# Performance work log

Hardware: AMD Instinct MI355X
Metric: run time of the kernel (lower is better)

## Reference

```python
import jax, jax.numpy as jnp
import numpy as np

SCALE = 8.0  # sqrt(d_head=64)

def setup_inputs() -> dict:
    key = jax.random.key(0)
    kq, kk, kv = jax.random.split(key, 3)
    B, H, S, D = 2, 16, 2048, 64
    q = jax.random.normal(kq, (B, H, S, D), dtype=jnp.float32)
    k = jax.random.normal(kk, (B, H, S, D), dtype=jnp.float32)
    v = jax.random.normal(kv, (B, H, S, D), dtype=jnp.float32)
    return {"q": q, "k": k, "v": v}

def reference(q, k, v):
    # attn = softmax((q/scale) @ k^T, axis=-1); out = attn @ v
    scores = jnp.einsum('bhqd,bhkd->bhqk', q / SCALE, k)  # [B,H,S,S]
    attn = jax.nn.softmax(scores, axis=-1)
    out = jnp.einsum('bhqk,bhkd->bhqd', attn, v)          # [B,H,S,D]
    return (attn, out)
```

## Files before the change

### kernel.cpp

```cpp
#include <hip/hip_runtime.h>


#define S_LEN 2048
#define D_HEAD 64
#define QB 64
#define KB 128
#define NCHUNK (S_LEN / KB)
#define KPAD 72
#define PPAD 136
#define ATTN_ELEMS 134217728ull
#define LOG2E 1.44269504088896340736f

#define WSE_KHI 0ull
#define WSE_KLO 4194304ull
#define WSE_VT  8388608ull
#define WSE_RINV 12582912ull
#define WS_NEEDED_BYTES (12582912ull * 2ull + 65536ull * 4ull)

typedef short short8 __attribute__((ext_vector_type(8)));
typedef _Float16 half8 __attribute__((ext_vector_type(8)));
typedef float f32x16 __attribute__((ext_vector_type(16)));
typedef float floatx4 __attribute__((ext_vector_type(4)));
typedef unsigned short ushort8v __attribute__((ext_vector_type(8)));

#if __has_builtin(__builtin_amdgcn_exp2f)
#define EXP2F(x) __builtin_amdgcn_exp2f(x)
#else
#define EXP2F(x) exp2f(x)
#endif

static __device__ __forceinline__ unsigned short f2bf(float f) {
  unsigned u = __builtin_bit_cast(unsigned, f);
  u += 0x7fffu + ((u >> 16) & 1u);
  return (unsigned short)(u >> 16);
}
static __device__ __forceinline__ float bf2f(unsigned short h) {
  unsigned u = ((unsigned)h) << 16;
  return __builtin_bit_cast(float, u);
}
static __device__ __forceinline__ unsigned short f2h(float f) {
  return __builtin_bit_cast(unsigned short, (_Float16)f);
}

__global__ __launch_bounds__(512) void k_prep_k(
    const float* __restrict__ kin, unsigned short* __restrict__ khi,
    unsigned short* __restrict__ klo) {
  const size_t base = ((size_t)blockIdx.x * 512 + threadIdx.x) * 8;
  floatx4 a = *(const floatx4*)(kin + base);
  floatx4 b = *(const floatx4*)(kin + base + 4);
  ushort8v h, l;
#pragma unroll
  for (int j = 0; j < 4; ++j) {
    unsigned short ha = f2bf(a[j]); h[j] = ha; l[j] = f2bf(a[j] - bf2f(ha));
    unsigned short hb = f2bf(b[j]); h[4 + j] = hb; l[4 + j] = f2bf(b[j] - bf2f(hb));
  }
  *(ushort8v*)(khi + base) = h;
  *(ushort8v*)(klo + base) = l;
}

__global__ __launch_bounds__(512) void k_prep_v(
    const float* __restrict__ vin, unsigned short* __restrict__ vt) {
  __shared__ __align__(16) unsigned short T[64 * KPAD];
  const int tid = threadIdx.x;
  const int bh = blockIdx.x >> 3;
  const int part = blockIdx.x & 7;
  const float* V = vin + (size_t)bh * S_LEN * D_HEAD;
  unsigned short* Vt = vt + (size_t)bh * D_HEAD * S_LEN;

  const int kk_l = tid >> 3;
  const int d0 = (tid & 7) * 8;
  const int dd = tid >> 3;
  const int kb = (tid & 7) * 8;

  for (int t = part * 4; t < part * 4 + 4; ++t) {
    const int kk0 = t * 64;
    floatx4 a = *(const floatx4*)(V + (size_t)(kk0 + kk_l) * D_HEAD + d0);
    floatx4 b = *(const floatx4*)(V + (size_t)(kk0 + kk_l) * D_HEAD + d0 + 4);
#pragma unroll
    for (int j = 0; j < 4; ++j) {
      T[(d0 + j) * KPAD + kk_l] = f2h(a[j]);
      T[(d0 + 4 + j) * KPAD + kk_l] = f2h(b[j]);
    }
    __syncthreads();
    *(ushort8v*)(Vt + (size_t)dd * S_LEN + kk0 + kb) = *(const ushort8v*)&T[dd * KPAD + kb];
    __syncthreads();
  }
}

__global__ __launch_bounds__(512, 4) void k_rowsum_f(
    const float* __restrict__ q, const unsigned short* __restrict__ khi,
    const unsigned short* __restrict__ klo, float* __restrict__ rinv) {
  __shared__ float rsum_s[QB];
  const int tid = threadIdx.x;
  const int lane = tid & 63;
  const int wid = tid >> 6;
  const int rg = wid & 1, cg = wid >> 1;
  const int bxs = (blockIdx.x & 7) * 128 + (blockIdx.x >> 3);
  const int bh = bxs >> 5;
  const int qt = bxs & 31;

  const float* Q = q + (size_t)bh * S_LEN * D_HEAD;
  const unsigned short* KH = khi + (size_t)bh * S_LEN * D_HEAD;
  const unsigned short* KL = klo + (size_t)bh * S_LEN * D_HEAD;

  if (tid < QB) rsum_s[tid] = 0.0f;

  const int arow = qt * QB + rg * 32 + (lane & 31);
  const float* qp = Q + (size_t)arow * D_HEAD + ((lane >> 5) * 8);
  short8 ahi[4], alo[4];
#pragma unroll
  for (int ks = 0; ks < 4; ++ks) {
    floatx4 x0 = *(const floatx4*)(qp + ks * 16);
    floatx4 x1 = *(const floatx4*)(qp + ks * 16 + 4);
    ushort8v uh, ul;
#pragma unroll
    for (int j = 0; j < 4; ++j) {
      float xa = x0[j] * 0.125f; unsigned short ha = f2bf(xa);
      uh[j] = ha; ul[j] = f2bf(xa - bf2f(ha));
      float xb = x1[j] * 0.125f; unsigned short hb = f2bf(xb);
      uh[4 + j] = hb; ul[4 + j] = f2bf(xb - bf2f(hb));
    }
    ahi[ks] = __builtin_bit_cast(short8, uh);
    alo[ks] = __builtin_bit_cast(short8, ul);
  }

  float psum[16];
#pragma unroll
  for (int i = 0; i < 16; ++i) psum[i] = 0.0f;

  const size_t brow0 = (size_t)(cg * 32 + (lane & 31)) * D_HEAD + (lane >> 5) * 8;

  for (int ch = 0; ch < NCHUNK; ++ch) {
    const size_t cbase = (size_t)ch * KB * D_HEAD + brow0;
    f32x16 acc = {};
#pragma unroll
    for (int ks = 0; ks < 4; ++ks) {
      ushort8v bhu = *(const ushort8v*)(KH + cbase + ks * 16);
      ushort8v blu = *(const ushort8v*)(KL + cbase + ks * 16);
      short8 bh8 = __builtin_bit_cast(short8, bhu);
      short8 bl8 = __builtin_bit_cast(short8, blu);
      acc = __builtin_amdgcn_mfma_f32_32x32x16_bf16(alo[ks], bh8, acc, 0, 0, 0);
      acc = __builtin_amdgcn_mfma_f32_32x32x16_bf16(ahi[ks], bl8, acc, 0, 0, 0);
      acc = __builtin_amdgcn_mfma_f32_32x32x16_bf16(ahi[ks], bh8, acc, 0, 0, 0);
    }
#pragma unroll
    for (int i = 0; i < 16; ++i) psum[i] += EXP2F(acc[i] * LOG2E);
  }

#pragma unroll
  for (int off = 1; off < 32; off <<= 1) {
#pragma unroll
    for (int i = 0; i < 16; ++i) psum[i] += __shfl_xor(psum[i], off, 64);
  }
  if ((lane & 31) == 0) {
    const int rbase = rg * 32 + 4 * (lane >> 5);
#pragma unroll
    for (int i = 0; i < 16; ++i)
      atomicAdd(&rsum_s[rbase + (i & 3) + 8 * (i >> 2)], psum[i]);
  }
  __syncthreads();
  if (tid < QB)
    rinv[(size_t)bh * S_LEN + qt * QB + tid] = 1.0f / rsum_s[tid];
}

__global__ __launch_bounds__(512, 4) void k_attn_f(
    const float* __restrict__ q, const unsigned short* __restrict__ khi,
    const unsigned short* __restrict__ klo, const unsigned short* __restrict__ vt,
    const float* __restrict__ rinv, float* __restrict__ outbuf) {
  __shared__ __align__(16) unsigned short Pst[QB * PPAD];
  __shared__ float rinv_s[QB];

  const int tid = threadIdx.x;
  const int lane = tid & 63;
  const int wid = tid >> 6;
  const int rg = wid & 1, cg = wid >> 1;
  const int dg = (wid >> 1) & 1, kh = wid >> 2;
  const int bxs = (blockIdx.x & 7) * 128 + (blockIdx.x >> 3);
  const int bh = bxs >> 5;
  const int qt = bxs & 31;

  const float* Q = q + (size_t)bh * S_LEN * D_HEAD;
  const unsigned short* KH = khi + (size_t)bh * S_LEN * D_HEAD;
  const unsigned short* KL = klo + (size_t)bh * S_LEN * D_HEAD;
  const unsigned short* VT = vt + (size_t)bh * D_HEAD * S_LEN;
  float* attn_base = outbuf + (size_t)bh * S_LEN * S_LEN + (size_t)qt * QB * S_LEN;
  float* out_base = outbuf + ATTN_ELEMS + (size_t)bh * S_LEN * D_HEAD +
                    (size_t)qt * QB * D_HEAD;

  if (tid < QB) rinv_s[tid] = rinv[(size_t)bh * S_LEN + qt * QB + tid];

  const int arow = qt * QB + rg * 32 + (lane & 31);
  const float* qp = Q + (size_t)arow * D_HEAD + ((lane >> 5) * 8);
  short8 ahi[4], alo[4];
#pragma unroll
  for (int ks = 0; ks < 4; ++ks) {
    floatx4 x0 = *(const floatx4*)(qp + ks * 16);
    floatx4 x1 = *(const floatx4*)(qp + ks * 16 + 4);
    ushort8v uh, ul;
#pragma unroll
    for (int j = 0; j < 4; ++j) {
      float xa = x0[j] * 0.125f; unsigned short ha = f2bf(xa);
      uh[j] = ha; ul[j] = f2bf(xa - bf2f(ha));
      float xb = x1[j] * 0.125f; unsigned short hb = f2bf(xb);
      uh[4 + j] = hb; ul[4 + j] = f2bf(xb - bf2f(hb));
    }
    ahi[ks] = __builtin_bit_cast(short8, uh);
    alo[ks] = __builtin_bit_cast(short8, ul);
  }
  __syncthreads();

  floatx4 rvec[4];
  {
    const int rb = rg * 32 + 4 * (lane >> 5);
#pragma unroll
    for (int m = 0; m < 4; ++m) rvec[m] = *(const floatx4*)&rinv_s[rb + 8 * m];
  }

  f32x16 oacc = {};
  const size_t brow0 = (size_t)(cg * 32 + (lane & 31)) * D_HEAD + (lane >> 5) * 8;
  const int boff = (lane >> 5) * 8;

  for (int ch = 0; ch < NCHUNK; ++ch) {
    const int kk0 = ch * KB;
    f32x16 acc = {};
    const size_t cbase = (size_t)kk0 * D_HEAD + brow0;
#pragma unroll
    for (int ks = 0; ks < 4; ++ks) {
      ushort8v bhu = *(const ushort8v*)(KH + cbase + ks * 16);
      ushort8v blu = *(const ushort8v*)(KL + cbase + ks * 16);
      short8 bh8 = __builtin_bit_cast(short8, bhu);
      short8 bl8 = __builtin_bit_cast(short8, blu);
      acc = __builtin_amdgcn_mfma_f32_32x32x16_bf16(alo[ks], bh8, acc, 0, 0, 0);
      acc = __builtin_amdgcn_mfma_f32_32x32x16_bf16(ahi[ks], bl8, acc, 0, 0, 0);
      acc = __builtin_amdgcn_mfma_f32_32x32x16_bf16(ahi[ks], bh8, acc, 0, 0, 0);
    }
    {
      const int rbase = rg * 32 + 4 * (lane >> 5);
      const int colg = kk0 + cg * 32 + (lane & 31);
#pragma unroll
      for (int i = 0; i < 16; ++i) {
        float p = EXP2F(acc[i] * LOG2E);
        float at = p * rvec[i >> 2][i & 3];
        const int rl = rbase + (i & 3) + 8 * (i >> 2);
        __builtin_nontemporal_store(at, &attn_base[(size_t)rl * S_LEN + colg]);
        Pst[rl * PPAD + cg * 32 + (lane & 31)] = f2h(at);
      }
    }
    __syncthreads();
#pragma unroll
    for (int ks = 0; ks < 4; ++ks) {
      const int kofs = kh * 64 + ks * 16 + boff;
      ushort8v pu = *(const ushort8v*)&Pst[(rg * 32 + (lane & 31)) * PPAD + kofs];
      ushort8v vu = *(const ushort8v*)(VT + (size_t)(dg * 32 + (lane & 31)) * S_LEN + kk0 + kofs);
      oacc = __builtin_amdgcn_mfma_f32_32x32x16_f16(
          __builtin_bit_cast(half8, pu), __builtin_bit_cast(half8, vu), oacc, 0, 0, 0);
    }
    __syncthreads();
  }

  float* red = (float*)Pst;
  const int t4 = wid & 3;
  if (kh == 1) {
#pragma unroll
    for (int i = 0; i < 16; ++i) red[t4 * 1024 + i * 64 + lane] = oacc[i];
  }
  __syncthreads();
  if (kh == 0) {
#pragma unroll
    for (int i = 0; i < 16; ++i) oacc[i] += red[t4 * 1024 + i * 64 + lane];
    const int rbase = rg * 32 + 4 * (lane >> 5);
#pragma unroll
    for (int i = 0; i < 16; ++i) {
      const int rl = rbase + (i & 3) + 8 * (i >> 2);
      out_base[(size_t)rl * D_HEAD + dg * 32 + (lane & 31)] = oacc[i];
    }
  }
}

__global__ __launch_bounds__(512, 4) void k_rowsum(
    const float* __restrict__ q, const float* __restrict__ k,
    float* __restrict__ outbuf) {
  __shared__ __align__(16) unsigned short KhiS[KB * KPAD];
  __shared__ __align__(16) unsigned short KloS[KB * KPAD];
  __shared__ float rsum_s[QB];
  const int tid = threadIdx.x;
  const int lane = tid & 63;
  const int wid = tid >> 6;
  const int rg = wid & 1, cg = wid >> 1;
  const int bh = blockIdx.x >> 5;
  const int qt = blockIdx.x & 31;
  const float* Q = q + (size_t)bh * S_LEN * D_HEAD;
  const float* K = k + (size_t)bh * S_LEN * D_HEAD;
  float* rinv_out = outbuf + ATTN_ELEMS + (size_t)bh * S_LEN * D_HEAD +
                    (size_t)qt * QB * D_HEAD;
  if (tid < QB) rsum_s[tid] = 0.0f;
  const int arow = qt * QB + rg * 32 + (lane & 31);
  const float* qp = Q + (size_t)arow * D_HEAD + ((lane >> 5) * 8);
  short8 ahi[4], alo[4];
#pragma unroll
  for (int ks = 0; ks < 4; ++ks) {
    floatx4 x0 = *(const floatx4*)(qp + ks * 16);
    floatx4 x1 = *(const floatx4*)(qp + ks * 16 + 4);
    ushort8v uh, ul;
#pragma unroll
    for (int j = 0; j < 4; ++j) {
      float xa = x0[j] * 0.125f; unsigned short ha = f2bf(xa);
      uh[j] = ha; ul[j] = f2bf(xa - bf2f(ha));
      float xb = x1[j] * 0.125f; unsigned short hb = f2bf(xb);
      uh[4 + j] = hb; ul[4 + j] = f2bf(xb - bf2f(hb));
    }
    ahi[ks] = __builtin_bit_cast(short8, uh);
    alo[ks] = __builtin_bit_cast(short8, ul);
  }
  float psum[16];
#pragma unroll
  for (int i = 0; i < 16; ++i) psum[i] = 0.0f;
  const int srow = tid >> 2;
  const int scol = (tid & 3) * 16;
  const int bcol = cg * 32 + (lane & 31);
  const int boff = (lane >> 5) * 8;
  for (int ch = 0; ch < NCHUNK; ++ch) {
    const int kk0 = ch * KB;
    {
      const float* src = K + (size_t)(kk0 + srow) * D_HEAD + scol;
      floatx4 v0 = *(const floatx4*)(src);
      floatx4 v1 = *(const floatx4*)(src + 4);
      floatx4 v2 = *(const floatx4*)(src + 8);
      floatx4 v3 = *(const floatx4*)(src + 12);
      ushort8v h0, h1, l0, l1;
#pragma unroll
      for (int j = 0; j < 4; ++j) {
        unsigned short a0 = f2bf(v0[j]); h0[j] = a0; l0[j] = f2bf(v0[j] - bf2f(a0));
        unsigned short a1 = f2bf(v1[j]); h0[4+j] = a1; l0[4+j] = f2bf(v1[j] - bf2f(a1));
        unsigned short a2 = f2bf(v2[j]); h1[j] = a2; l1[j] = f2bf(v2[j] - bf2f(a2));
        unsigned short a3 = f2bf(v3[j]); h1[4+j] = a3; l1[4+j] = f2bf(v3[j] - bf2f(a3));
      }
      *(ushort8v*)&KhiS[srow * KPAD + scol] = h0;
      *(ushort8v*)&KhiS[srow * KPAD + scol + 8] = h1;
      *(ushort8v*)&KloS[srow * KPAD + scol] = l0;
      *(ushort8v*)&KloS[srow * KPAD + scol + 8] = l1;
    }
    __syncthreads();
    f32x16 acc = {};
#pragma unroll
    for (int ks = 0; ks < 4; ++ks) {
      ushort8v bhu = *(const ushort8v*)&KhiS[bcol * KPAD + ks * 16 + boff];
      ushort8v blu = *(const ushort8v*)&KloS[bcol * KPAD + ks * 16 + boff];
      short8 bh8 = __builtin_bit_cast(short8, bhu);
      short8 bl8 = __builtin_bit_cast(short8, blu);
      acc = __builtin_amdgcn_mfma_f32_32x32x16_bf16(alo[ks], bh8, acc, 0, 0, 0);
      acc = __builtin_amdgcn_mfma_f32_32x32x16_bf16(ahi[ks], bl8, acc, 0, 0, 0);
      acc = __builtin_amdgcn_mfma_f32_32x32x16_bf16(ahi[ks], bh8, acc, 0, 0, 0);
    }
#pragma unroll
    for (int i = 0; i < 16; ++i) psum[i] += EXP2F(acc[i] * LOG2E);
    __syncthreads();
  }
#pragma unroll
  for (int off = 1; off < 32; off <<= 1) {
#pragma unroll
    for (int i = 0; i < 16; ++i) psum[i] += __shfl_xor(psum[i], off, 64);
  }
  if ((lane & 31) == 0) {
    const int rbase = rg * 32 + 4 * (lane >> 5);
#pragma unroll
    for (int i = 0; i < 16; ++i)
      atomicAdd(&rsum_s[rbase + (i & 3) + 8 * (i >> 2)], psum[i]);
  }
  __syncthreads();
  if (tid < QB) rinv_out[tid] = 1.0f / rsum_s[tid];
}

__global__ __launch_bounds__(512, 4) void k_attn(
    const float* __restrict__ q, const float* __restrict__ k,
    const float* __restrict__ v, float* __restrict__ outbuf) {
  __shared__ __align__(16) unsigned short KhiS[KB * KPAD];
  __shared__ __align__(16) unsigned short KloS[KB * KPAD];
  __shared__ __align__(16) unsigned short Pst[QB * PPAD];
  __shared__ __align__(16) unsigned short VtS[D_HEAD * PPAD];
  __shared__ float rinv_s[QB];
  const int tid = threadIdx.x;
  const int lane = tid & 63;
  const int wid = tid >> 6;
  const int rg = wid & 1, cg = wid >> 1;
  const int dg = (wid >> 1) & 1, kh = wid >> 2;
  const int bh = blockIdx.x >> 5;
  const int qt = blockIdx.x & 31;
  const float* Q = q + (size_t)bh * S_LEN * D_HEAD;
  const float* K = k + (size_t)bh * S_LEN * D_HEAD;
  const float* V = v + (size_t)bh * S_LEN * D_HEAD;
  float* attn_base = outbuf + (size_t)bh * S_LEN * S_LEN + (size_t)qt * QB * S_LEN;
  float* out_base = outbuf + ATTN_ELEMS + (size_t)bh * S_LEN * D_HEAD +
                    (size_t)qt * QB * D_HEAD;
  if (tid < QB) rinv_s[tid] = out_base[tid];
  const int arow = qt * QB + rg * 32 + (lane & 31);
  const float* qp = Q + (size_t)arow * D_HEAD + ((lane >> 5) * 8);
  short8 ahi[4], alo[4];
#pragma unroll
  for (int ks = 0; ks < 4; ++ks) {
    floatx4 x0 = *(const floatx4*)(qp + ks * 16);
    floatx4 x1 = *(const floatx4*)(qp + ks * 16 + 4);
    ushort8v uh, ul;
#pragma unroll
    for (int j = 0; j < 4; ++j) {
      float xa = x0[j] * 0.125f; unsigned short ha = f2bf(xa);
      uh[j] = ha; ul[j] = f2bf(xa - bf2f(ha));
      float xb = x1[j] * 0.125f; unsigned short hb = f2bf(xb);
      uh[4 + j] = hb; ul[4 + j] = f2bf(xb - bf2f(hb));
    }
    ahi[ks] = __builtin_bit_cast(short8, uh);
    alo[ks] = __builtin_bit_cast(short8, ul);
  }
  __syncthreads();
  floatx4 rvec[4];
  {
    const int rb = rg * 32 + 4 * (lane >> 5);
#pragma unroll
    for (int m = 0; m < 4; ++m) rvec[m] = *(const floatx4*)&rinv_s[rb + 8 * m];
  }
  f32x16 oacc = {};
  const int srow = tid >> 2;
  const int scol = (tid & 3) * 16;
  const int bcol = cg * 32 + (lane & 31);
  const int boff = (lane >> 5) * 8;
  for (int ch = 0; ch < NCHUNK; ++ch) {
    const int kk0 = ch * KB;
    {
      const float* src = K + (size_t)(kk0 + srow) * D_HEAD + scol;
      floatx4 v0 = *(const floatx4*)(src);
      floatx4 v1 = *(const floatx4*)(src + 4);
      floatx4 v2 = *(const floatx4*)(src + 8);
      floatx4 v3 = *(const floatx4*)(src + 12);
      ushort8v h0, h1, l0, l1;
#pragma unroll
      for (int j = 0; j < 4; ++j) {
        unsigned short a0 = f2bf(v0[j]); h0[j] = a0; l0[j] = f2bf(v0[j] - bf2f(a0));
        unsigned short a1 = f2bf(v1[j]); h0[4+j] = a1; l0[4+j] = f2bf(v1[j] - bf2f(a1));
        unsigned short a2 = f2bf(v2[j]); h1[j] = a2; l1[j] = f2bf(v2[j] - bf2f(a2));
        unsigned short a3 = f2bf(v3[j]); h1[4+j] = a3; l1[4+j] = f2bf(v3[j] - bf2f(a3));
      }
      *(ushort8v*)&KhiS[srow * KPAD + scol] = h0;
      *(ushort8v*)&KhiS[srow * KPAD + scol + 8] = h1;
      *(ushort8v*)&KloS[srow * KPAD + scol] = l0;
      *(ushort8v*)&KloS[srow * KPAD + scol + 8] = l1;
    }
    {
#pragma unroll
      for (int half = 0; half < 2; ++half) {
        const float* vsrc = V + (size_t)(kk0 + half * 64 + wid * 8) * D_HEAD + lane;
        ushort8v hv;
#pragma unroll
        for (int i = 0; i < 8; ++i) hv[i] = f2h(vsrc[(size_t)i * D_HEAD]);
        *(ushort8v*)&VtS[lane * PPAD + half * 64 + wid * 8] = hv;
      }
    }
    __syncthreads();
    f32x16 acc = {};
#pragma unroll
    for (int ks = 0; ks < 4; ++ks) {
      ushort8v bhu = *(const ushort8v*)&KhiS[bcol * KPAD + ks * 16 + boff];
      ushort8v blu = *(const ushort8v*)&KloS[bcol * KPAD + ks * 16 + boff];
      short8 bh8 = __builtin_bit_cast(short8, bhu);
      short8 bl8 = __builtin_bit_cast(short8, blu);
      acc = __builtin_amdgcn_mfma_f32_32x32x16_bf16(alo[ks], bh8, acc, 0, 0, 0);
      acc = __builtin_amdgcn_mfma_f32_32x32x16_bf16(ahi[ks], bl8, acc, 0, 0, 0);
      acc = __builtin_amdgcn_mfma_f32_32x32x16_bf16(ahi[ks], bh8, acc, 0, 0, 0);
    }
    {
      const int rbase = rg * 32 + 4 * (lane >> 5);
      const int colg = kk0 + cg * 32 + (lane & 31);
#pragma unroll
      for (int i = 0; i < 16; ++i) {
        float p = EXP2F(acc[i] * LOG2E);
        float at = p * rvec[i >> 2][i & 3];
        const int rl = rbase + (i & 3) + 8 * (i >> 2);
        __builtin_nontemporal_store(at, &attn_base[(size_t)rl * S_LEN + colg]);
        Pst[rl * PPAD + cg * 32 + (lane & 31)] = f2h(at);
      }
    }
    __syncthreads();
#pragma unroll
    for (int ks = 0; ks < 4; ++ks) {
      const int kofs = kh * 64 + ks * 16 + boff;
      ushort8v pu = *(const ushort8v*)&Pst[(rg * 32 + (lane & 31)) * PPAD + kofs];
      ushort8v vu = *(const ushort8v*)&VtS[(dg * 32 + (lane & 31)) * PPAD + kofs];
      oacc = __builtin_amdgcn_mfma_f32_32x32x16_f16(
          __builtin_bit_cast(half8, pu), __builtin_bit_cast(half8, vu), oacc, 0, 0, 0);
    }
    __syncthreads();
  }
  float* red = (float*)KhiS;
  const int t4 = wid & 3;
  if (kh == 1) {
#pragma unroll
    for (int i = 0; i < 16; ++i) red[t4 * 1024 + i * 64 + lane] = oacc[i];
  }
  __syncthreads();
  if (kh == 0) {
#pragma unroll
    for (int i = 0; i < 16; ++i) oacc[i] += red[t4 * 1024 + i * 64 + lane];
    const int rbase = rg * 32 + 4 * (lane >> 5);
#pragma unroll
    for (int i = 0; i < 16; ++i) {
      const int rl = rbase + (i & 3) + 8 * (i >> 2);
      out_base[(size_t)rl * D_HEAD + dg * 32 + (lane & 31)] = oacc[i];
    }
  }
}

extern "C" void kernel_launch(void* const* d_in, const int* in_sizes, int n_in,
                              void* d_out, int out_size, void* d_ws, size_t ws_size,
                              hipStream_t stream) {
  const float* q = (const float*)d_in[0];
  const float* k = (const float*)d_in[1];
  const float* v = (const float*)d_in[2];
  float* out = (float*)d_out;
  (void)in_sizes; (void)n_in; (void)out_size;

  dim3 blk(512);
  if (ws_size >= WS_NEEDED_BYTES) {
    unsigned short* wsu = (unsigned short*)d_ws;
    unsigned short* khi = wsu + WSE_KHI;
    unsigned short* klo = wsu + WSE_KLO;
    unsigned short* vt = wsu + WSE_VT;
    float* rinv = (float*)(wsu + WSE_RINV);
    hipLaunchKernelGGL(k_prep_k, dim3(1024), blk, 0, stream, k, khi, klo);
    hipLaunchKernelGGL(k_prep_v, dim3(256), blk, 0, stream, v, vt);
    hipLaunchKernelGGL(k_rowsum_f, dim3(1024), blk, 0, stream, q, khi, klo, rinv);
    hipLaunchKernelGGL(k_attn_f, dim3(1024), blk, 0, stream, q, khi, klo, vt, rinv, out);
  } else {
    hipLaunchKernelGGL(k_rowsum, dim3(1024), blk, 0, stream, q, k, out);
    hipLaunchKernelGGL(k_attn, dim3(1024), blk, 0, stream, q, k, v, out);
  }
}
```

Before: 829.0 us.

## Fuse rowsum into attention kernel, merge prep kernels, use fragment-ordered K/V layouts

Merges the K and V preparation kernels into one launch and folds the row-sum pass into the attention kernel, so the attention kernel computes its own softmax normalizers before the main pass and the rinv workspace goes away. K hi/lo and V-transpose are stored in an MFMA-fragment-major layout, so each lane reads contiguous 16-byte pieces. P staging is double-buffered in shared memory, which removes one barrier per chunk and lets the attn stores overlap the PV MFMAs. This cuts launch count and workspace traffic, at the cost of more LDS per block, which could lower occupancy.

```diff
diff --git a/kernel.cpp b/kernel.cpp
--- a/kernel.cpp
+++ b/kernel.cpp
@@ -10,12 +10,12 @@
 #define PPAD 136
 #define ATTN_ELEMS 134217728ull
 #define LOG2E 1.44269504088896340736f
+#define HFRAG 131072ull
 
 #define WSE_KHI 0ull
 #define WSE_KLO 4194304ull
 #define WSE_VT  8388608ull
-#define WSE_RINV 12582912ull
-#define WS_NEEDED_BYTES (12582912ull * 2ull + 65536ull * 4ull)
+#define WS_NEEDED_BYTES (12582912ull * 2ull)
 
 typedef short short8 __attribute__((ext_vector_type(8)));
 typedef _Float16 half8 __attribute__((ext_vector_type(8)));
@@ -42,133 +42,77 @@
   return __builtin_bit_cast(unsigned short, (_Float16)f);
 }
 
-__global__ __launch_bounds__(512) void k_prep_k(
-    const float* __restrict__ kin, unsigned short* __restrict__ khi,
-    unsigned short* __restrict__ klo) {
-  const size_t base = ((size_t)blockIdx.x * 512 + threadIdx.x) * 8;
-  floatx4 a = *(const floatx4*)(kin + base);
-  floatx4 b = *(const floatx4*)(kin + base + 4);
-  ushort8v h, l;
-#pragma unroll
-  for (int j = 0; j < 4; ++j) {
-    unsigned short ha = f2bf(a[j]); h[j] = ha; l[j] = f2bf(a[j] - bf2f(ha));
-    unsigned short hb = f2bf(b[j]); h[4 + j] = hb; l[4 + j] = f2bf(b[j] - bf2f(hb));
-  }
-  *(ushort8v*)(khi + base) = h;
-  *(ushort8v*)(klo + base) = l;
-}
-
-__global__ __launch_bounds__(512) void k_prep_v(
-    const float* __restrict__ vin, unsigned short* __restrict__ vt) {
-  __shared__ __align__(16) unsigned short T[64 * KPAD];
+__global__ __launch_bounds__(512) void k_prep(
+    const float* __restrict__ kin, const float* __restrict__ vin,
+    unsigned short* __restrict__ khi, unsigned short* __restrict__ klo,
+    unsigned short* __restrict__ vt) {
+  __shared__ __align__(16) unsigned short T[64 * PPAD];
   const int tid = threadIdx.x;
-  const int bh = blockIdx.x >> 3;
-  const int part = blockIdx.x & 7;
-  const float* V = vin + (size_t)bh * S_LEN * D_HEAD;
-  unsigned short* Vt = vt + (size_t)bh * D_HEAD * S_LEN;
-
-  const int kk_l = tid >> 3;
-  const int d0 = (tid & 7) * 8;
-  const int dd = tid >> 3;
-  const int kb = (tid & 7) * 8;
-
-  for (int t = part * 4; t < part * 4 + 4; ++t) {
-    const int kk0 = t * 64;
-    floatx4 a = *(const floatx4*)(V + (size_t)(kk0 + kk_l) * D_HEAD + d0);
-    floatx4 b = *(const floatx4*)(V + (size_t)(kk0 + kk_l) * D_HEAD + d0 + 4);
+  const int b = blockIdx.x;
+  if (b < 512) {
+    const int bh = b >> 4, ch = b & 15;
+    const int srow = tid >> 2;
+    const int ks = tid & 3;
+    const int d0 = ks * 16;
+    const float* src = kin + ((size_t)bh * S_LEN + ch * KB + srow) * D_HEAD + d0;
+    floatx4 v0 = *(const floatx4*)(src);
+    floatx4 v1 = *(const floatx4*)(src + 4);
+    floatx4 v2 = *(const floatx4*)(src + 8);
+    floatx4 v3 = *(const floatx4*)(src + 12);
+    ushort8v h0, h1, l0, l1;
 #pragma unroll
     for (int j = 0; j < 4; ++j) {
-      T[(d0 + j) * KPAD + kk_l] = f2h(a[j]);
-      T[(d0 + 4 + j) * KPAD + kk_l] = f2h(b[j]);
-    }
-    __syncthreads();
-    *(ushort8v*)(Vt + (size_t)dd * S_LEN + kk0 + kb) = *(const ushort8v*)&T[dd * KPAD + kb];
-    __syncthreads();
-  }
-}
-
-__global__ __launch_bounds__(512, 4) void k_rowsum_f(
-    const float* __restrict__ q, const unsigned short* __restrict__ khi,
-    const unsigned short* __restrict__ klo, float* __restrict__ rinv) {
-  __shared__ float rsum_s[QB];
-  const int tid = threadIdx.x;
-  const int lane = tid & 63;
-  const int wid = tid >> 6;
-  const int rg = wid & 1, cg = wid >> 1;
-  const int bxs = (blockIdx.x & 7) * 128 + (blockIdx.x >> 3);
-  const int bh = bxs >> 5;
-  const int qt = bxs & 31;
-
-  const float* Q = q + (size_t)bh * S_LEN * D_HEAD;
-  const unsigned short* KH = khi + (size_t)bh * S_LEN * D_HEAD;
-  const unsigned short* KL = klo + (size_t)bh * S_LEN * D_HEAD;
-
-  if (tid < QB) rsum_s[tid] = 0.0f;
-
-  const int arow = qt * QB + rg * 32 + (lane & 31);
-  const float* qp = Q + (size_t)arow * D_HEAD + ((lane >> 5) * 8);
-  short8 ahi[4], alo[4];
-#pragma unroll
-  for (int ks = 0; ks < 4; ++ks) {
-    floatx4 x0 = *(const floatx4*)(qp + ks * 16);
-    floatx4 x1 = *(const floatx4*)(qp + ks * 16 + 4);
-    ushort8v uh, ul;
+      unsigned short a0 = f2bf(v0[j]); h0[j] = a0; l0[j] = f2bf(v0[j] - bf2f(a0));
+      unsigned short a1 = f2bf(v1[j]); h0[4+j] = a1; l0[4+j] = f2bf(v1[j] - bf2f(a1));
+      unsigned short a2 = f2bf(v2[j]); h1[j] = a2; l1[j] = f2bf(v2[j] - bf2f(a2));
+      unsigned short a3 = f2bf(v3[j]); h1[4+j] = a3; l1[4+j] = f2bf(v3[j] - bf2f(a3));
+    }
+    const int cg = srow >> 5, r = srow & 31;
+    const size_t base = (size_t)bh * HFRAG +
+                        ((size_t)(ch * 4 + cg) * 2048 + (size_t)ks * 512);
+    *(ushort8v*)(khi + base + r * 8) = h0;
+    *(ushort8v*)(khi + base + (32 + r) * 8) = h1;
+    *(ushort8v*)(klo + base + r * 8) = l0;
+    *(ushort8v*)(klo + base + (32 + r) * 8) = l1;
+  } else {
+    const int bb = b - 512;
+    const int bh = bb >> 4, ch = bb & 15;
+    const int srow = tid >> 2;
+    const int d0 = (tid & 3) * 16;
+    const float* src = vin + ((size_t)bh * S_LEN + ch * KB + srow) * D_HEAD + d0;
+    floatx4 v0 = *(const floatx4*)(src);
+    floatx4 v1 = *(const floatx4*)(src + 4);
+    floatx4 v2 = *(const floatx4*)(src + 8);
+    floatx4 v3 = *(const floatx4*)(src + 12);
 #pragma unroll
     for (int j = 0; j < 4; ++j) {
-      float xa = x0[j] * 0.125f; unsigned short ha = f2bf(xa);
-      uh[j] = ha; ul[j] = f2bf(xa - bf2f(ha));
-      float xb = x1[j] * 0.125f; unsigned short hb = f2bf(xb);
-      uh[4 + j] = hb; ul[4 + j] = f2bf(xb - bf2f(hb));
-    }
-    ahi[ks] = __builtin_bit_cast(short8, uh);
-    alo[ks] = __builtin_bit_cast(short8, ul);
-  }
-
-  float psum[16];
-#pragma unroll
-  for (int i = 0; i < 16; ++i) psum[i] = 0.0f;
-
-  const size_t brow0 = (size_t)(cg * 32 + (lane & 31)) * D_HEAD + (lane >> 5) * 8;
-
-  for (int ch = 0; ch < NCHUNK; ++ch) {
-    const size_t cbase = (size_t)ch * KB * D_HEAD + brow0;
-    f32x16 acc = {};
-#pragma unroll
-    for (int ks = 0; ks < 4; ++ks) {
-      ushort8v bhu = *(const ushort8v*)(KH + cbase + ks * 16);
-      ushort8v blu = *(const ushort8v*)(KL + cbase + ks * 16);
-      short8 bh8 = __builtin_bit_cast(short8, bhu);
-      short8 bl8 = __builtin_bit_cast(short8, blu);
-      acc = __builtin_amdgcn_mfma_f32_32x32x16_bf16(alo[ks], bh8, acc, 0, 0, 0);
-      acc = __builtin_amdgcn_mfma_f32_32x32x16_bf16(ahi[ks], bl8, acc, 0, 0, 0);
-      acc = __builtin_amdgcn_mfma_f32_32x32x16_bf16(ahi[ks], bh8, acc, 0, 0, 0);
-    }
-#pragma unroll
-    for (int i = 0; i < 16; ++i) psum[i] += EXP2F(acc[i] * LOG2E);
-  }
-
-#pragma unroll
-  for (int off = 1; off < 32; off <<= 1) {
-#pragma unroll
-    for (int i = 0; i < 16; ++i) psum[i] += __shfl_xor(psum[i], off, 64);
-  }
-  if ((lane & 31) == 0) {
-    const int rbase = rg * 32 + 4 * (lane >> 5);
-#pragma unroll
-    for (int i = 0; i < 16; ++i)
-      atomicAdd(&rsum_s[rbase + (i & 3) + 8 * (i >> 2)], psum[i]);
-  }
-  __syncthreads();
-  if (tid < QB)
-    rinv[(size_t)bh * S_LEN + qt * QB + tid] = 1.0f / rsum_s[tid];
-}
-
-__global__ __launch_bounds__(512, 4) void k_attn_f(
+      T[(d0 + j) * PPAD + srow] = f2h(v0[j]);
+      T[(d0 + 4 + j) * PPAD + srow] = f2h(v1[j]);
+      T[(d0 + 8 + j) * PPAD + srow] = f2h(v2[j]);
+      T[(d0 + 12 + j) * PPAD + srow] = f2h(v3[j]);
+    }
+    __syncthreads();
+    const size_t obase = (size_t)bh * HFRAG + (size_t)ch * 8192;
+#pragma unroll
+    for (int pp = 0; pp < 2; ++pp) {
+      const int p = tid * 2 + pp;
+      const int pl = p & 63;
+      const int ks2 = (p >> 6) & 3;
+      const int dg2 = (p >> 8) & 1;
+      const int kh2 = (p >> 9) & 1;
+      const int rowd = dg2 * 32 + (pl & 31);
+      const int kkl = kh2 * 64 + ks2 * 16 + (pl >> 5) * 8;
+      *(ushort8v*)(vt + obase + (size_t)p * 8) = *(const ushort8v*)&T[rowd * PPAD + kkl];
+    }
+  }
+}
+
+__global__ __launch_bounds__(512, 4) void k_fused(
     const float* __restrict__ q, const unsigned short* __restrict__ khi,
     const unsigned short* __restrict__ klo, const unsigned short* __restrict__ vt,
-    const float* __restrict__ rinv, float* __restrict__ outbuf) {
-  __shared__ __align__(16) unsigned short Pst[QB * PPAD];
-  __shared__ float rinv_s[QB];
+    float* __restrict__ outbuf) {
+  __shared__ __align__(16) unsigned short Pst[2][QB * PPAD];
+  __shared__ float rsum_s[QB];
 
   const int tid = threadIdx.x;
   const int lane = tid & 63;
@@ -180,14 +124,13 @@
   const int qt = bxs & 31;
 
   const float* Q = q + (size_t)bh * S_LEN * D_HEAD;
-  const unsigned short* KH = khi + (size_t)bh * S_LEN * D_HEAD;
-  const unsigned short* KL = klo + (size_t)bh * S_LEN * D_HEAD;
-  const unsigned short* VT = vt + (size_t)bh * D_HEAD * S_LEN;
+  const unsigned short* KHb = khi + (size_t)bh * HFRAG;
+  const unsigned short* KLb = klo + (size_t)bh * HFRAG;
+  const unsigned short* VTb = vt + (size_t)bh * HFRAG;
   float* attn_base = outbuf + (size_t)bh * S_LEN * S_LEN + (size_t)qt * QB * S_LEN;
-  float* out_base = outbuf + ATTN_ELEMS + (size_t)bh * S_LEN * D_HEAD +
-                    (size_t)qt * QB * D_HEAD;
-
-  if (tid < QB) rinv_s[tid] = rinv[(size_t)bh * S_LEN + qt * QB + tid];
+  float* out_base = outbuf + ATTN_ELEMS + ((size_t)bh * S_LEN + qt * QB) * D_HEAD;
+
+  if (tid < QB) rsum_s[tid] = 0.0f;
 
   const int arow = qt * QB + rg * 32 + (lane & 31);
   const float* qp = Q + (size_t)arow * D_HEAD + ((lane >> 5) * 8);
@@ -209,56 +152,90 @@
   }
   __syncthreads();
 
+  float psum[16];
+#pragma unroll
+  for (int i = 0; i < 16; ++i) psum[i] = 0.0f;
+
+  for (int ch = 0; ch < NCHUNK; ++ch) {
+    const size_t off = (size_t)(ch * 4 + cg) * 2048 + (size_t)lane * 8;
+    f32x16 acc = {};
+#pragma unroll
+    for (int ks = 0; ks < 4; ++ks) {
+      short8 bh8 = __builtin_bit_cast(short8, *(const ushort8v*)(KHb + off + ks * 512));
+      short8 bl8 = __builtin_bit_cast(short8, *(const ushort8v*)(KLb + off + ks * 512));
+      acc = __builtin_amdgcn_mfma_f32_32x32x16_bf16(alo[ks], bh8, acc, 0, 0, 0);
+      acc = __builtin_amdgcn_mfma_f32_32x32x16_bf16(ahi[ks], bl8, acc, 0, 0, 0);
+      acc = __builtin_amdgcn_mfma_f32_32x32x16_bf16(ahi[ks], bh8, acc, 0, 0, 0);
+    }
+#pragma unroll
+    for (int i = 0; i < 16; ++i) psum[i] += EXP2F(acc[i] * LOG2E);
+  }
+
+#pragma unroll
+  for (int off = 1; off < 32; off <<= 1) {
+#pragma unroll
+    for (int i = 0; i < 16; ++i) psum[i] += __shfl_xor(psum[i], off, 64);
+  }
+  if ((lane & 31) == 0) {
+    const int rbase = rg * 32 + 4 * (lane >> 5);
+#pragma unroll
+    for (int i = 0; i < 16; ++i)
+      atomicAdd(&rsum_s[rbase + (i & 3) + 8 * (i >> 2)], psum[i]);
+  }
+  __syncthreads();
+  if (tid < QB) rsum_s[tid] = 1.0f / rsum_s[tid];
+  __syncthreads();
+
   floatx4 rvec[4];
   {
     const int rb = rg * 32 + 4 * (lane >> 5);
 #pragma unroll
-    for (int m = 0; m < 4; ++m) rvec[m] = *(const floatx4*)&rinv_s[rb + 8 * m];
+    for (int m = 0; m < 4; ++m) rvec[m] = *(const floatx4*)&rsum_s[rb + 8 * m];
   }
 
   f32x16 oacc = {};
-  const size_t brow0 = (size_t)(cg * 32 + (lane & 31)) * D_HEAD + (lane >> 5) * 8;
   const int boff = (lane >> 5) * 8;
+  const int rbase = rg * 32 + 4 * (lane >> 5);
+  const int colb = cg * 32 + (lane & 31);
 
   for (int ch = 0; ch < NCHUNK; ++ch) {
-    const int kk0 = ch * KB;
+    const size_t off = (size_t)(ch * 4 + cg) * 2048 + (size_t)lane * 8;
     f32x16 acc = {};
-    const size_t cbase = (size_t)kk0 * D_HEAD + brow0;
 #pragma unroll
     for (int ks = 0; ks < 4; ++ks) {
-      ushort8v bhu = *(const ushort8v*)(KH + cbase + ks * 16);
-      ushort8v blu = *(const ushort8v*)(KL + cbase + ks * 16);
-      short8 bh8 = __builtin_bit_cast(short8, bhu);
-      short8 bl8 = __builtin_bit_cast(short8, blu);
+      short8 bh8 = __builtin_bit_cast(short8, *(const ushort8v*)(KHb + off + ks * 512));
+      short8 bl8 = __builtin_bit_cast(short8, *(const ushort8v*)(KLb + off + ks * 512));
       acc = __builtin_amdgcn_mfma_f32_32x32x16_bf16(alo[ks], bh8, acc, 0, 0, 0);
       acc = __builtin_amdgcn_mfma_f32_32x32x16_bf16(ahi[ks], bl8, acc, 0, 0, 0);
       acc = __builtin_amdgcn_mfma_f32_32x32x16_bf16(ahi[ks], bh8, acc, 0, 0, 0);
     }
+    unsigned short* PB = &Pst[ch & 1][0];
+#pragma unroll
+    for (int i = 0; i < 16; ++i) {
+      acc[i] = EXP2F(acc[i] * LOG2E) * rvec[i >> 2][i & 3];
+      PB[(rbase + (i & 3) + 8 * (i >> 2)) * PPAD + colb] = f2h(acc[i]);
+    }
+    __syncthreads();
     {
-      const int rbase = rg * 32 + 4 * (lane >> 5);
-      const int colg = kk0 + cg * 32 + (lane & 31);
+      const int colg = ch * KB + colb;
 #pragma unroll
       for (int i = 0; i < 16; ++i) {
-        float p = EXP2F(acc[i] * LOG2E);
-        float at = p * rvec[i >> 2][i & 3];
         const int rl = rbase + (i & 3) + 8 * (i >> 2);
-        __builtin_nontemporal_store(at, &attn_base[(size_t)rl * S_LEN + colg]);
-        Pst[rl * PPAD + cg * 32 + (lane & 31)] = f2h(at);
+        __builtin_nontemporal_store(acc[i], &attn_base[(size_t)rl * S_LEN + colg]);
       }
     }
-    __syncthreads();
 #pragma unroll
     for (int ks = 0; ks < 4; ++ks) {
       const int kofs = kh * 64 + ks * 16 + boff;
-      ushort8v pu = *(const ushort8v*)&Pst[(rg * 32 + (lane & 31)) * PPAD + kofs];
-      ushort8v vu = *(const ushort8v*)(VT + (size_t)(dg * 32 + (lane & 31)) * S_LEN + kk0 + kofs);
+      ushort8v pu = *(const ushort8v*)&PB[(rg * 32 + (lane & 31)) * PPAD + kofs];
+      ushort8v vu = *(const ushort8v*)(VTb + (size_t)ch * 8192 +
+                                       ((size_t)((kh * 2 + dg) * 4 + ks) * 64 + lane) * 8);
       oacc = __builtin_amdgcn_mfma_f32_32x32x16_f16(
           __builtin_bit_cast(half8, pu), __builtin_bit_cast(half8, vu), oacc, 0, 0, 0);
     }
-    __syncthreads();
-  }
-
-  float* red = (float*)Pst;
+  }
+
+  float* red = (float*)&Pst[0][0];
   const int t4 = wid & 3;
   if (kh == 1) {
 #pragma unroll
@@ -268,7 +245,6 @@
   if (kh == 0) {
 #pragma unroll
     for (int i = 0; i < 16; ++i) oacc[i] += red[t4 * 1024 + i * 64 + lane];
-    const int rbase = rg * 32 + 4 * (lane >> 5);
 #pragma unroll
     for (int i = 0; i < 16; ++i) {
       const int rl = rbase + (i & 3) + 8 * (i >> 2);
@@ -523,11 +499,8 @@
     unsigned short* khi = wsu + WSE_KHI;
     unsigned short* klo = wsu + WSE_KLO;
     unsigned short* vt = wsu + WSE_VT;
-    float* rinv = (float*)(wsu + WSE_RINV);
-    hipLaunchKernelGGL(k_prep_k, dim3(1024), blk, 0, stream, k, khi, klo);
-    hipLaunchKernelGGL(k_prep_v, dim3(256), blk, 0, stream, v, vt);
-    hipLaunchKernelGGL(k_rowsum_f, dim3(1024), blk, 0, stream, q, khi, klo, rinv);
-    hipLaunchKernelGGL(k_attn_f, dim3(1024), blk, 0, stream, q, khi, klo, vt, rinv, out);
+    hipLaunchKernelGGL(k_prep, dim3(1024), blk, 0, stream, k, v, khi, klo, vt);
+    hipLaunchKernelGGL(k_fused, dim3(1024), blk, 0, stream, q, khi, klo, vt, out);
   } else {
     hipLaunchKernelGGL(k_rowsum, dim3(1024), blk, 0, stream, q, k, out);
     hipLaunchKernelGGL(k_attn, dim3(1024), blk, 0, stream, q, k, v, out);
```

Result: faster. 708.2 us (-14.6%).
